# Performance work log

Measured on AMD Instinct MI355X. Metric: run time of the kernel, lower is better.

## Reference

```python
import math
import jax, jax.numpy as jnp
import numpy as np

NUM_HEADS = 16


def setup_inputs() -> dict:
    key = jax.random.key(0)
    ks = jax.random.split(key, 5)
    B, S, D = 2, 2048, 1024
    return {
        "x": jax.random.normal(ks[0], (B, S, D), dtype=jnp.float32),
        "w_in": jax.random.normal(ks[1], (3 * D, D), dtype=jnp.float32) * (1.0 / math.sqrt(D)),
        "b_in": jax.random.normal(ks[2], (3 * D,), dtype=jnp.float32) * 0.02,
        "w_out": jax.random.normal(ks[3], (D, D), dtype=jnp.float32) * (1.0 / math.sqrt(D)),
        "b_out": jax.random.normal(ks[4], (D,), dtype=jnp.float32) * 0.02,
        "causal_mask": 1,
    }


def reference(x, w_in, b_in, w_out, b_out, causal_mask):
    B, S, D = x.shape
    H = NUM_HEADS
    dh = D // H
    # in-projection: torch Linear -> x @ W^T + b, then chunk into q,k,v
    qkv = x @ w_in.T + b_in                      # [B,S,3D]
    q, k, v = jnp.split(qkv, 3, axis=-1)         # each [B,S,D]
    q = q.reshape(B, S, H, dh).transpose(0, 2, 1, 3)  # [B,H,S,dh]
    k = k.reshape(B, S, H, dh).transpose(0, 2, 1, 3)
    v = v.reshape(B, S, H, dh).transpose(0, 2, 1, 3)
    # NOTE: original computes k @ q^T => scores indexed [key, query]
    scores = jnp.einsum("bhkd,bhqd->bhkq", k, q) / math.sqrt(dh)  # [B,H,Sk,Sq]
    if causal_mask:
        # triu(1) on the [k,q] matrix: mask where q_index > k_index
        mask = jnp.triu(jnp.ones((S, S), dtype=bool), 1)
        scores = jnp.where(mask, -jnp.inf, scores)
    att = jax.nn.softmax(scores, axis=-1)        # softmax over query axis (faithful)
    out = jnp.einsum("bhkq,bhqd->bhkd", att, v)  # [B,H,S,dh]
    out = out.transpose(0, 2, 1, 3).reshape(B, S, D)
    return out @ w_out.T + b_out
```

## Files before the change

### kernel.cpp

```cpp
#include <hip/hip_runtime.h>

typedef unsigned short u16;
typedef short bfrag __attribute__((ext_vector_type(8)));
typedef float facc  __attribute__((ext_vector_type(4)));
typedef float f16x  __attribute__((ext_vector_type(16)));

__device__ __forceinline__ u16 f2bf(float f){
  union { float f; unsigned u; } v; v.f = f;
  unsigned r = v.u + 0x7fffu + ((v.u >> 16) & 1u);
  return (u16)(r >> 16);
}

__device__ __forceinline__ unsigned cvt_pk_bf16(float lo, float hi){
  unsigned d;
  asm("v_cvt_pk_bf16_f32 %0, %1, %2" : "=v"(d) : "v"(lo), "v"(hi));
  return d;
}

__device__ __forceinline__ void gl_lds16(const void* g, void* l){
  __builtin_amdgcn_global_load_lds(
      (const __attribute__((address_space(1))) unsigned int*)g,
      (__attribute__((address_space(3))) unsigned int*)l,
      16, 0, 0);
}

__global__ __launch_bounds__(256) void cvt3_kernel(
    const float* __restrict__ s0, u16* __restrict__ d0, int n0,
    const float* __restrict__ s1, u16* __restrict__ d1, int n1,
    const float* __restrict__ s2, u16* __restrict__ d2)
{
  int i = (blockIdx.x * 256 + threadIdx.x) * 4;
  const float* src; u16* dst;
  if (i < n0){ src = s0; dst = d0; }
  else if (i < n0 + n1){ src = s1; dst = d1; i -= n0; }
  else { src = s2; dst = d2; i -= n0 + n1; }
  float4 f = *(const float4*)(src + i);
  ushort4 o;
  o.x = f2bf(f.x); o.y = f2bf(f.y); o.z = f2bf(f.z); o.w = f2bf(f.w);
  *(ushort4*)(dst + i) = o;
}

__global__ __launch_bounds__(512, 2) void gemm8p_qkv(
    const u16* __restrict__ A, const u16* __restrict__ B,
    const float* __restrict__ bias, u16* __restrict__ qkv)
{
  __shared__ u16 lds[66048];
  const int tid = threadIdx.x, lane = tid & 63;
  const int w = tid >> 6, wm = w >> 2, wn = w & 3;
  const int cl = lane & 15, g8 = (lane >> 4) * 8, r0 = (lane >> 4) * 4;
  constexpr int K = 1024, NT = 16;

  const int bid = blockIdx.x;
  const int chunk = bid & 7, pos = bid >> 3;
  const int mt = (chunk >> 2) * 8 + pos / 3;
  const int nt = (chunk & 3) * 3 + pos % 3;
  const int m0 = mt * 256, n0 = nt * 256;

  facc acc[8][4];
  #pragma unroll
  for (int mi = 0; mi < 8; ++mi)
    #pragma unroll
    for (int ni = 0; ni < 4; ++ni) acc[mi][ni] = (facc){0.f, 0.f, 0.f, 0.f};

  int aoff[4][2], boff[2][2];
  #pragma unroll
  for (int mi2 = 0; mi2 < 4; ++mi2)
    #pragma unroll
    for (int ks = 0; ks < 2; ++ks){
      int r = (2 * mi2 + wm) * 16 + cl;
      int U = r * 128 + (ks * 32 + g8) * 2;
      aoff[mi2][ks] = (U ^ (((U >> 9) & 1) << 5)) >> 1;
    }
  #pragma unroll
  for (int ni2 = 0; ni2 < 2; ++ni2)
    #pragma unroll
    for (int ks = 0; ks < 2; ++ks){
      int rB = (4 * ni2 + wn) * 16 + cl;
      int U = rB * 128 + (ks * 32 + g8) * 2;
      boff[ni2][ks] = (U ^ (((U >> 9) & 1) << 5)) >> 1;
    }

  int srow[2], scol[2];
  #pragma unroll
  for (int c = 0; c < 2; ++c){
    int Bh = c * 8192 + tid * 16;
    int E = Bh ^ (((Bh >> 9) & 1) << 5);
    srow[c] = E >> 7; scol[c] = (E & 127) >> 1;
  }

  auto stageA = [&](int t, int h){
    const int k0 = (t < NT) ? t * 64 : 0;
    const int slot = ((2 * t + h) & 3) * 8192;
    #pragma unroll
    for (int c = 0; c < 2; ++c)
      gl_lds16(A + (size_t)(m0 + h * 128 + srow[c]) * K + k0 + scol[c],
               lds + slot + c * 4096 + w * 512);
  };
  auto stageB = [&](int t, int h){
    const int k0 = (t < NT) ? t * 64 : 0;
    const int slot = 32768 + ((2 * t + h) & 3) * 8192;
    #pragma unroll
    for (int c = 0; c < 2; ++c)
      gl_lds16(B + (size_t)(n0 + h * 128 + srow[c]) * K + k0 + scol[c],
               lds + slot + c * 4096 + w * 512);
  };

  stageA(0, 0); stageB(0, 0); stageA(0, 1); stageB(0, 1); stageA(1, 0); stageB(1, 0);

  bfrag af[4][2], bf[2][2];

  for (int j = 0; j < NT; ++j){
    const int sa0 = ((2 * j) & 3) * 8192,      sa1 = ((2 * j + 1) & 3) * 8192;
    const int sb0 = 32768 + ((2 * j) & 3) * 8192, sb1 = 32768 + ((2 * j + 1) & 3) * 8192;

    stageA(j + 1, 1);
    asm volatile("s_waitcnt vmcnt(8)" ::: "memory");
    __builtin_amdgcn_s_barrier();
    #pragma unroll
    for (int mi2 = 0; mi2 < 4; ++mi2)
      #pragma unroll
      for (int ks = 0; ks < 2; ++ks) af[mi2][ks] = *(const bfrag*)&lds[sa0 + aoff[mi2][ks]];
    #pragma unroll
    for (int ni2 = 0; ni2 < 2; ++ni2)
      #pragma unroll
      for (int ks = 0; ks < 2; ++ks) bf[ni2][ks] = *(const bfrag*)&lds[sb0 + boff[ni2][ks]];
    asm volatile("s_waitcnt lgkmcnt(0)" ::: "memory");
    __builtin_amdgcn_sched_barrier(0);
    __builtin_amdgcn_s_setprio(1);
    #pragma unroll
    for (int mi2 = 0; mi2 < 4; ++mi2)
      #pragma unroll
      for (int ni2 = 0; ni2 < 2; ++ni2)
        #pragma unroll
        for (int ks = 0; ks < 2; ++ks)
          acc[mi2][ni2] = __builtin_amdgcn_mfma_f32_16x16x32_bf16(af[mi2][ks], bf[ni2][ks], acc[mi2][ni2], 0, 0, 0);
    __builtin_amdgcn_s_setprio(0);
    __builtin_amdgcn_s_barrier();

    stageB(j + 1, 1);
    asm volatile("s_waitcnt vmcnt(6)" ::: "memory");
    __builtin_amdgcn_s_barrier();
    #pragma unroll
    for (int ni2 = 0; ni2 < 2; ++ni2)
      #pragma unroll
      for (int ks = 0; ks < 2; ++ks) bf[ni2][ks] = *(const bfrag*)&lds[sb1 + boff[ni2][ks]];
    asm volatile("s_waitcnt lgkmcnt(0)" ::: "memory");
    __builtin_amdgcn_sched_barrier(0);
    __builtin_amdgcn_s_setprio(1);
    #pragma unroll
    for (int mi2 = 0; mi2 < 4; ++mi2)
      #pragma unroll
      for (int ni2 = 0; ni2 < 2; ++ni2)
        #pragma unroll
        for (int ks = 0; ks < 2; ++ks)
          acc[mi2][2 + ni2] = __builtin_amdgcn_mfma_f32_16x16x32_bf16(af[mi2][ks], bf[ni2][ks], acc[mi2][2 + ni2], 0, 0, 0);
    __builtin_amdgcn_s_setprio(0);
    __builtin_amdgcn_s_barrier();

    #pragma unroll
    for (int mi2 = 0; mi2 < 4; ++mi2)
      #pragma unroll
      for (int ks = 0; ks < 2; ++ks) af[mi2][ks] = *(const bfrag*)&lds[sa1 + aoff[mi2][ks]];
    #pragma unroll
    for (int ni2 = 0; ni2 < 2; ++ni2)
      #pragma unroll
      for (int ks = 0; ks < 2; ++ks) bf[ni2][ks] = *(const bfrag*)&lds[sb0 + boff[ni2][ks]];
    stageA(j + 2, 0);
    __builtin_amdgcn_s_barrier();
    asm volatile("s_waitcnt lgkmcnt(0)" ::: "memory");
    __builtin_amdgcn_sched_barrier(0);
    __builtin_amdgcn_s_setprio(1);
    #pragma unroll
    for (int mi2 = 0; mi2 < 4; ++mi2)
      #pragma unroll
      for (int ni2 = 0; ni2 < 2; ++ni2)
        #pragma unroll
        for (int ks = 0; ks < 2; ++ks)
          acc[4 + mi2][ni2] = __builtin_amdgcn_mfma_f32_16x16x32_bf16(af[mi2][ks], bf[ni2][ks], acc[4 + mi2][ni2], 0, 0, 0);
    __builtin_amdgcn_s_setprio(0);
    __builtin_amdgcn_s_barrier();

    #pragma unroll
    for (int ni2 = 0; ni2 < 2; ++ni2)
      #pragma unroll
      for (int ks = 0; ks < 2; ++ks) bf[ni2][ks] = *(const bfrag*)&lds[sb1 + boff[ni2][ks]];
    stageB(j + 2, 0);
    __builtin_amdgcn_s_barrier();
    asm volatile("s_waitcnt lgkmcnt(0)" ::: "memory");
    __builtin_amdgcn_sched_barrier(0);
    __builtin_amdgcn_s_setprio(1);
    #pragma unroll
    for (int mi2 = 0; mi2 < 4; ++mi2)
      #pragma unroll
      for (int ni2 = 0; ni2 < 2; ++ni2)
        #pragma unroll
        for (int ks = 0; ks < 2; ++ks)
          acc[4 + mi2][2 + ni2] = __builtin_amdgcn_mfma_f32_16x16x32_bf16(af[mi2][ks], bf[ni2][ks], acc[4 + mi2][2 + ni2], 0, 0, 0);
    __builtin_amdgcn_s_setprio(0);
    __builtin_amdgcn_s_barrier();
  }
  __syncthreads();

  const int bb = m0 >> 11, s0q = m0 & 2047;
  if (n0 < 2048){
    #pragma unroll
    for (int mi = 0; mi < 8; ++mi){
      const int m = m0 + (2 * mi + wm) * 16 + r0;
      #pragma unroll
      for (int ni = 0; ni < 4; ++ni){
        const int n = n0 + (4 * ni + wn) * 16 + cl;
        const float bv = bias[n];
        const int part = n >> 10, rest = n & 1023;
        const int h = rest >> 6, d = rest & 63;
        #pragma unroll
        for (int jj = 0; jj < 4; ++jj){
          float v = acc[mi][ni][jj] + bv;
          if (part == 0) v *= 0.18033688011112042f;
          const int mm = m + jj;
          qkv[(size_t)part * 4194304 + (size_t)(((mm >> 11) * 16 + h) * 2048 + (mm & 2047)) * 64 + d] = f2bf(v);
        }
      }
    }
  } else {
    u16* tr = lds;
    const int h0 = (n0 - 2048) >> 6;
    #pragma unroll
    for (int mi = 0; mi < 8; ++mi){
      const int sl = (2 * mi + wm) * 16 + r0;
      #pragma unroll
      for (int ni = 0; ni < 4; ++ni){
        const float bv = bias[n0 + (4 * ni + wn) * 16 + cl];
        const int off = (ni * 64 + wn * 16 + cl) * 258 + sl;
        *(unsigned*)&tr[off]     = cvt_pk_bf16(acc[mi][ni][0] + bv, acc[mi][ni][1] + bv);
        *(unsigned*)&tr[off + 2] = cvt_pk_bf16(acc[mi][ni][2] + bv, acc[mi][ni][3] + bv);
      }
    }
    __syncthreads();
    u16* vt_base = qkv + (size_t)2 * 4194304;
    const int hh = tid >> 7, dd = (tid >> 1) & 63, hf = tid & 1;
    u16* dst = vt_base + ((size_t)((bb * 16 + h0 + hh) * 64 + dd)) * 2048 + s0q + hf * 128;
    const u16* srcr = &tr[(hh * 64 + dd) * 258 + hf * 128];
    #pragma unroll
    for (int k = 0; k < 16; ++k)
      *(uint4*)(dst + k * 8) = *(const uint4*)(srcr + k * 8);
  }
}

__device__ __forceinline__ void stage_tile(const u16* __restrict__ G, u16* lds,
                                           int row0, int k0, int K, int tid){
  #pragma unroll
  for (int c = 0; c < 2; ++c){
    int e = c * 2048 + tid * 8;
    int row = e >> 5, col = e & 31;
    gl_lds16(G + (size_t)(row0 + row) * K + k0 + col, lds + c * 2048 + (tid >> 6) * 512);
  }
}

__global__ __launch_bounds__(256) void gemm_out(
    const u16* __restrict__ A, const u16* __restrict__ B,
    const float* __restrict__ bias, float* __restrict__ Cf,
    int M, int N, int K)
{
  __shared__ u16 smem[16384];
  u16* Ash = smem;
  u16* Bsh = smem + 8192;
  const int tid = threadIdx.x, lane = tid & 63;
  const int w = tid >> 6, wm = w >> 1, wn = w & 1;
  const int cl = lane & 15, g8 = (lane >> 4) * 8;

  const int bid = blockIdx.x;
  const int chunk = bid & 7, pos = bid >> 3;
  const int mt = (chunk >> 1) * 8 + pos / 4;
  const int nt = (chunk & 1) * 4 + pos % 4;
  const int n0 = nt * 128, m0 = mt * 128;

  facc acc[4][4];
  #pragma unroll
  for (int mi = 0; mi < 4; ++mi)
    #pragma unroll
    for (int ni = 0; ni < 4; ++ni)
      acc[mi][ni] = (facc){0.f, 0.f, 0.f, 0.f};

  const int NT = K >> 5;
  stage_tile(A, Ash, m0, 0, K, tid);
  stage_tile(B, Bsh, n0, 0, K, tid);
  __syncthreads();
  int cur = 0;
  for (int kt = 0; kt < NT; ++kt){
    if (kt + 1 < NT){
      stage_tile(A, Ash + (cur ^ 1) * 4096, m0, (kt + 1) << 5, K, tid);
      stage_tile(B, Bsh + (cur ^ 1) * 4096, n0, (kt + 1) << 5, K, tid);
    }
    const u16* As = Ash + cur * 4096; const u16* Bs = Bsh + cur * 4096;
    bfrag af[4], bfr[4];
    #pragma unroll
    for (int mi = 0; mi < 4; ++mi)
      af[mi] = *(const bfrag*)&As[(wm * 64 + mi * 16 + cl) * 32 + g8];
    #pragma unroll
    for (int ni = 0; ni < 4; ++ni)
      bfr[ni] = *(const bfrag*)&Bs[(wn * 64 + ni * 16 + cl) * 32 + g8];
    #pragma unroll
    for (int mi = 0; mi < 4; ++mi)
      #pragma unroll
      for (int ni = 0; ni < 4; ++ni)
        acc[mi][ni] = __builtin_amdgcn_mfma_f32_16x16x32_bf16(af[mi], bfr[ni], acc[mi][ni], 0, 0, 0);
    __syncthreads();
    cur ^= 1;
  }

  const int r0 = (lane >> 4) * 4;
  #pragma unroll
  for (int mi = 0; mi < 4; ++mi){
    const int mbase = m0 + wm * 64 + mi * 16 + r0;
    #pragma unroll
    for (int ni = 0; ni < 4; ++ni){
      const int n = n0 + wn * 64 + ni * 16 + cl;
      const float bv = bias[n];
      #pragma unroll
      for (int j = 0; j < 4; ++j)
        Cf[(size_t)(mbase + j) * N + n] = acc[mi][ni][j] + bv;
    }
  }
}

template<int NSUB, bool MASK>
__device__ __forceinline__ void attn_tile(
    const u16* __restrict__ Kt, const u16* __restrict__ VTh, int jt,
    int il, int hi, const bfrag (&bq)[4],
    f16x& o0, f16x& o1, float& m_s, float& l_s)
{
  bfrag vf[NSUB * 4];
  #pragma unroll
  for (int sub = 0; sub < NSUB; ++sub)
    #pragma unroll
    for (int half = 0; half < 2; ++half){
      const int jcol = jt * 64 + sub * 32 + half * 16 + hi * 8;
      vf[sub * 4 + half * 2 + 0] = *(const bfrag*)(VTh + (size_t)il * 2048 + jcol);
      vf[sub * 4 + half * 2 + 1] = *(const bfrag*)(VTh + (size_t)(32 + il) * 2048 + jcol);
    }
  bfrag kf[NSUB * 4];
  #pragma unroll
  for (int sub = 0; sub < NSUB; ++sub)
    #pragma unroll
    for (int kt = 0; kt < 4; ++kt)
      kf[sub * 4 + kt] = *(const bfrag*)(Kt + (size_t)(sub * 32 + il) * 64 + kt * 16 + hi * 8);

  f16x s[NSUB];
  #pragma unroll
  for (int sub = 0; sub < NSUB; ++sub)
    #pragma unroll
    for (int r = 0; r < 16; ++r) s[sub][r] = 0.f;
  __builtin_amdgcn_s_setprio(1);
  #pragma unroll
  for (int kt = 0; kt < 4; ++kt)
    #pragma unroll
    for (int sub = 0; sub < NSUB; ++sub)
      s[sub] = __builtin_amdgcn_mfma_f32_32x32x16_bf16(kf[sub * 4 + kt], bq[kt], s[sub], 0, 0, 0);
  __builtin_amdgcn_s_setprio(0);

  if (MASK){
    #pragma unroll
    for (int r = 0; r < 16; ++r){
      const int qj = (r & 3) + 8 * (r >> 2) + 4 * hi;
      if (qj > il) s[NSUB - 1][r] = -1e30f;
    }
  }

  float tmax = -1e30f;
  #pragma unroll
  for (int sub = 0; sub < NSUB; ++sub){
    float a[8];
    #pragma unroll
    for (int e = 0; e < 8; ++e) a[e] = fmaxf(s[sub][e], s[sub][e + 8]);
    #pragma unroll
    for (int e = 0; e < 4; ++e) a[e] = fmaxf(a[e], a[e + 4]);
    a[0] = fmaxf(fmaxf(a[0], a[2]), fmaxf(a[1], a[3]));
    tmax = fmaxf(tmax, a[0]);
  }
  {
    auto tt = __builtin_amdgcn_permlane32_swap(__float_as_uint(tmax),
                                               __float_as_uint(tmax), false, false);
    tmax = fmaxf(__uint_as_float(tt[0]), __uint_as_float(tt[1]));
  }
  if (__any(tmax - m_s > 8.0f)){
    const float nm = fmaxf(m_s, tmax);
    const float sc = __builtin_amdgcn_exp2f(m_s - nm);
    m_s = nm; l_s *= sc;
    #pragma unroll
    for (int r = 0; r < 16; ++r){
      const float scb = __shfl(sc, (r & 3) + 8 * (r >> 2) + 4 * hi, 64);
      o0[r] *= scb; o1[r] *= scb;
    }
  }

  float rsum = 0.f;
  #pragma unroll
  for (int sub = 0; sub < NSUB; ++sub){
    #pragma unroll
    for (int r = 0; r < 16; ++r)
      s[sub][r] = __builtin_amdgcn_exp2f(s[sub][r] - m_s);
    float a[8];
    #pragma unroll
    for (int e = 0; e < 8; ++e) a[e] = s[sub][e] + s[sub][e + 8];
    #pragma unroll
    for (int e = 0; e < 4; ++e) a[e] = a[e] + a[e + 4];
    rsum += (a[0] + a[2]) + (a[1] + a[3]);
  }
  {
    auto rr = __builtin_amdgcn_permlane32_swap(__float_as_uint(rsum),
                                               __float_as_uint(rsum), false, false);
    rsum = __uint_as_float(rr[0]) + __uint_as_float(rr[1]);
  }
  l_s += rsum;

  #pragma unroll
  for (int sub = 0; sub < NSUB; ++sub)
    #pragma unroll
    for (int half = 0; half < 2; ++half){
      const int q0 = 8 * half;
      unsigned a0 = cvt_pk_bf16(s[sub][q0],     s[sub][q0 + 1]);
      unsigned a1 = cvt_pk_bf16(s[sub][q0 + 2], s[sub][q0 + 3]);
      unsigned b0 = cvt_pk_bf16(s[sub][q0 + 4], s[sub][q0 + 5]);
      unsigned b1 = cvt_pk_bf16(s[sub][q0 + 6], s[sub][q0 + 7]);
      auto r0p = __builtin_amdgcn_permlane32_swap(a0, b0, false, false);
      auto r1p = __builtin_amdgcn_permlane32_swap(a1, b1, false, false);
      union { bfrag f; unsigned u[4]; } pa;
      pa.u[0] = r0p[0]; pa.u[1] = r1p[0]; pa.u[2] = r0p[1]; pa.u[3] = r1p[1];

      __builtin_amdgcn_s_setprio(1);
      o0 = __builtin_amdgcn_mfma_f32_32x32x16_bf16(pa.f, vf[sub * 4 + half * 2 + 0], o0, 0, 0, 0);
      o1 = __builtin_amdgcn_mfma_f32_32x32x16_bf16(pa.f, vf[sub * 4 + half * 2 + 1], o1, 0, 0, 0);
      __builtin_amdgcn_s_setprio(0);
    }
}

__global__ __launch_bounds__(128, 3) void attn_kernel(
    const u16* __restrict__ qarr, const u16* __restrict__ karr,
    const u16* __restrict__ vtarr, u16* __restrict__ aout,
    const int* __restrict__ cmask)
{
  __shared__ float cO[32 * 64];
  __shared__ float cm0[32], cl0[32], cm1[32], cl1[32];
  const int tid = threadIdx.x, lane = tid & 63, w = tid >> 6;
  const int il = lane & 31, hi = lane >> 5;
  const int bh = blockIdx.x;
  const int jw = 63 - (int)blockIdx.y;
  const int iw = jw * 32;
  const u16* Qh  = karr  + (size_t)bh * 131072;
  const u16* Kh  = qarr  + (size_t)bh * 131072;
  const u16* VTh = vtarr + (size_t)bh * 131072;
  const bool do_mask = (cmask[0] != 0);

  bfrag bq[4];
  #pragma unroll
  for (int kt = 0; kt < 4; ++kt)
    bq[kt] = *(const bfrag*)(Qh + (size_t)(iw + il) * 64 + kt * 16 + hi * 8);

  f16x o0, o1;
  #pragma unroll
  for (int r = 0; r < 16; ++r){ o0[r] = 0.f; o1[r] = 0.f; }
  float m_s = -1e30f, l_s = 0.f;

  const int my_diag = jw >> 1;
  const int dsub    = jw & 1;
  const int lim = do_mask ? my_diag : 32;

  for (int jt = w; jt < lim; jt += 2)
    attn_tile<2, false>(Kh + (size_t)jt * 4096, VTh, jt, il, hi, bq, o0, o1, m_s, l_s);

  if (do_mask && (my_diag & 1) == w){
    if (dsub == 0)
      attn_tile<1, true>(Kh + (size_t)my_diag * 4096, VTh, my_diag, il, hi, bq, o0, o1, m_s, l_s);
    else
      attn_tile<2, true>(Kh + (size_t)my_diag * 4096, VTh, my_diag, il, hi, bq, o0, o1, m_s, l_s);
  }

  if (w == 1){
    #pragma unroll
    for (int r = 0; r < 16; ++r){
      const int row = (r & 3) + 8 * (r >> 2) + 4 * hi;
      cO[row * 64 + il]      = o0[r];
      cO[row * 64 + il + 32] = o1[r];
    }
    cm1[il] = m_s; cl1[il] = l_s;
  } else {
    cm0[il] = m_s; cl0[il] = l_s;
  }
  __syncthreads();
  if (w == 0){
    const int bb = bh >> 4, h = bh & 15;
    #pragma unroll
    for (int r = 0; r < 16; ++r){
      const int rl = (r & 3) + 8 * (r >> 2) + 4 * hi;
      const float mA = cm0[rl], mB = cm1[rl];
      const float lA = cl0[rl], lB = cl1[rl];
      const float M  = fmaxf(mA, mB);
      const float eA = __builtin_amdgcn_exp2f(mA - M);
      const float eB = __builtin_amdgcn_exp2f(mB - M);
      const float inv = 1.0f / (lA * eA + lB * eB);
      const float ob0 = cO[rl * 64 + il], ob1 = cO[rl * 64 + il + 32];
      u16* dst = aout + (size_t)(bb * 2048 + iw + rl) * 1024 + h * 64 + il;
      dst[0]  = f2bf((o0[r] * eA + ob0 * eB) * inv);
      dst[32] = f2bf((o1[r] * eA + ob1 * eB) * inv);
    }
  }
}

extern "C" void kernel_launch(void* const* d_in, const int* in_sizes, int n_in,
                              void* d_out, int out_size, void* d_ws, size_t ws_size,
                              hipStream_t stream)
{
  const float* x     = (const float*)d_in[0];
  const float* w_in  = (const float*)d_in[1];
  const float* b_in  = (const float*)d_in[2];
  const float* w_out = (const float*)d_in[3];
  const float* b_out = (const float*)d_in[4];
  const int*   cmask = (const int*)d_in[5];

  u16* ws     = (u16*)d_ws;
  u16* xb     = ws;
  u16* winb   = ws + 4194304;
  u16* woutb  = ws + 7340032;
  u16* qs     = ws + 8388608;
  u16* attn_o = ws + 20971520;

  cvt3_kernel<<<8192, 256, 0, stream>>>(x, xb, 4194304,
                                        w_in, winb, 3145728,
                                        w_out, woutb);

  gemm8p_qkv<<<192, 512, 0, stream>>>(xb, winb, b_in, qs);

  attn_kernel<<<dim3(32, 64), 128, 0, stream>>>(qs, qs + 4194304, qs + 8388608, attn_o, cmask);

  gemm_out<<<256, 256, 0, stream>>>(attn_o, woutb, b_out, (float*)d_out,
                                    4096, 1024, 1024);
}
```

Before: 146.9 us.

## Process two 32-row query stripes per attention block to reuse K/V fragments

Each attention block now handles 64 query rows, split into two 32-row stripes, instead of 32. Each K/V tile is loaded into registers once and used by both stripes, so global K/V traffic per query row is halved. The grid shrinks to 32x32 blocks, launch bounds are dropped, and register and LDS use per block grow, which may cut occupancy and parallelism. Causal load balance is also coarser, since each block's work now scales in 64-row steps.

```diff
diff --git a/kernel.cpp b/kernel.cpp
--- a/kernel.cpp
+++ b/kernel.cpp
@@ -110,7 +110,7 @@
   bfrag af[4][2], bf[2][2];
 
   for (int j = 0; j < NT; ++j){
-    const int sa0 = ((2 * j) & 3) * 8192,      sa1 = ((2 * j + 1) & 3) * 8192;
+    const int sa0 = ((2 * j) & 3) * 8192,         sa1 = ((2 * j + 1) & 3) * 8192;
     const int sb0 = 32768 + ((2 * j) & 3) * 8192, sb1 = 32768 + ((2 * j + 1) & 3) * 8192;
 
     stageA(j + 1, 1);
@@ -324,27 +324,11 @@
 }
 
 template<int NSUB, bool MASK>
-__device__ __forceinline__ void attn_tile(
-    const u16* __restrict__ Kt, const u16* __restrict__ VTh, int jt,
+__device__ __forceinline__ void stripe_body(
+    const bfrag (&kf)[8], const bfrag (&vf)[8],
     int il, int hi, const bfrag (&bq)[4],
     f16x& o0, f16x& o1, float& m_s, float& l_s)
 {
-  bfrag vf[NSUB * 4];
-  #pragma unroll
-  for (int sub = 0; sub < NSUB; ++sub)
-    #pragma unroll
-    for (int half = 0; half < 2; ++half){
-      const int jcol = jt * 64 + sub * 32 + half * 16 + hi * 8;
-      vf[sub * 4 + half * 2 + 0] = *(const bfrag*)(VTh + (size_t)il * 2048 + jcol);
-      vf[sub * 4 + half * 2 + 1] = *(const bfrag*)(VTh + (size_t)(32 + il) * 2048 + jcol);
-    }
-  bfrag kf[NSUB * 4];
-  #pragma unroll
-  for (int sub = 0; sub < NSUB; ++sub)
-    #pragma unroll
-    for (int kt = 0; kt < 4; ++kt)
-      kf[sub * 4 + kt] = *(const bfrag*)(Kt + (size_t)(sub * 32 + il) * 64 + kt * 16 + hi * 8);
-
   f16x s[NSUB];
   #pragma unroll
   for (int sub = 0; sub < NSUB; ++sub)
@@ -434,74 +418,104 @@
     }
 }
 
-__global__ __launch_bounds__(128, 3) void attn_kernel(
+__device__ __forceinline__ void load_tile(
+    bfrag (&kf)[8], bfrag (&vf)[8],
+    const u16* __restrict__ Kt, const u16* __restrict__ VTh, int jt, int il, int hi)
+{
+  #pragma unroll
+  for (int sub = 0; sub < 2; ++sub)
+    #pragma unroll
+    for (int half = 0; half < 2; ++half){
+      const int jcol = jt * 64 + sub * 32 + half * 16 + hi * 8;
+      vf[sub * 4 + half * 2 + 0] = *(const bfrag*)(VTh + (size_t)il * 2048 + jcol);
+      vf[sub * 4 + half * 2 + 1] = *(const bfrag*)(VTh + (size_t)(32 + il) * 2048 + jcol);
+    }
+  #pragma unroll
+  for (int sub = 0; sub < 2; ++sub)
+    #pragma unroll
+    for (int kt = 0; kt < 4; ++kt)
+      kf[sub * 4 + kt] = *(const bfrag*)(Kt + (size_t)(sub * 32 + il) * 64 + kt * 16 + hi * 8);
+}
+
+__global__ void attn_kernel(
     const u16* __restrict__ qarr, const u16* __restrict__ karr,
     const u16* __restrict__ vtarr, u16* __restrict__ aout,
     const int* __restrict__ cmask)
 {
-  __shared__ float cO[32 * 64];
-  __shared__ float cm0[32], cl0[32], cm1[32], cl1[32];
+  __shared__ float cO[64 * 64];
+  __shared__ float cm0[64], cl0[64], cm1[64], cl1[64];
   const int tid = threadIdx.x, lane = tid & 63, w = tid >> 6;
   const int il = lane & 31, hi = lane >> 5;
   const int bh = blockIdx.x;
-  const int jw = 63 - (int)blockIdx.y;
-  const int iw = jw * 32;
+  const int bi = 31 - (int)blockIdx.y;
+  const int i0 = bi * 64;
   const u16* Qh  = karr  + (size_t)bh * 131072;
   const u16* Kh  = qarr  + (size_t)bh * 131072;
   const u16* VTh = vtarr + (size_t)bh * 131072;
   const bool do_mask = (cmask[0] != 0);
 
-  bfrag bq[4];
-  #pragma unroll
-  for (int kt = 0; kt < 4; ++kt)
-    bq[kt] = *(const bfrag*)(Qh + (size_t)(iw + il) * 64 + kt * 16 + hi * 8);
-
-  f16x o0, o1;
-  #pragma unroll
-  for (int r = 0; r < 16; ++r){ o0[r] = 0.f; o1[r] = 0.f; }
-  float m_s = -1e30f, l_s = 0.f;
-
-  const int my_diag = jw >> 1;
-  const int dsub    = jw & 1;
-  const int lim = do_mask ? my_diag : 32;
-
-  for (int jt = w; jt < lim; jt += 2)
-    attn_tile<2, false>(Kh + (size_t)jt * 4096, VTh, jt, il, hi, bq, o0, o1, m_s, l_s);
-
-  if (do_mask && (my_diag & 1) == w){
-    if (dsub == 0)
-      attn_tile<1, true>(Kh + (size_t)my_diag * 4096, VTh, my_diag, il, hi, bq, o0, o1, m_s, l_s);
-    else
-      attn_tile<2, true>(Kh + (size_t)my_diag * 4096, VTh, my_diag, il, hi, bq, o0, o1, m_s, l_s);
+  bfrag bqL[4], bqH[4];
+  #pragma unroll
+  for (int kt = 0; kt < 4; ++kt){
+    bqL[kt] = *(const bfrag*)(Qh + (size_t)(i0 + il) * 64 + kt * 16 + hi * 8);
+    bqH[kt] = *(const bfrag*)(Qh + (size_t)(i0 + 32 + il) * 64 + kt * 16 + hi * 8);
+  }
+
+  f16x o0L, o1L, o0H, o1H;
+  #pragma unroll
+  for (int r = 0; r < 16; ++r){ o0L[r] = 0.f; o1L[r] = 0.f; o0H[r] = 0.f; o1H[r] = 0.f; }
+  float mL = -1e30f, lL = 0.f, mH = -1e30f, lH = 0.f;
+
+  const int lim = do_mask ? bi : 32;
+
+  bfrag kf[8], vf[8];
+  for (int jt = w; jt < lim; jt += 2){
+    load_tile(kf, vf, Kh + (size_t)jt * 4096, VTh, jt, il, hi);
+    stripe_body<2, false>(kf, vf, il, hi, bqL, o0L, o1L, mL, lL);
+    stripe_body<2, false>(kf, vf, il, hi, bqH, o0H, o1H, mH, lH);
+  }
+
+  if (do_mask && (bi & 1) == w){
+    load_tile(kf, vf, Kh + (size_t)bi * 4096, VTh, bi, il, hi);
+    stripe_body<1, true>(kf, vf, il, hi, bqL, o0L, o1L, mL, lL);
+    stripe_body<2, true>(kf, vf, il, hi, bqH, o0H, o1H, mH, lH);
   }
 
   if (w == 1){
     #pragma unroll
     for (int r = 0; r < 16; ++r){
       const int row = (r & 3) + 8 * (r >> 2) + 4 * hi;
-      cO[row * 64 + il]      = o0[r];
-      cO[row * 64 + il + 32] = o1[r];
-    }
-    cm1[il] = m_s; cl1[il] = l_s;
+      cO[row * 64 + il]             = o0L[r];
+      cO[row * 64 + il + 32]        = o1L[r];
+      cO[(32 + row) * 64 + il]      = o0H[r];
+      cO[(32 + row) * 64 + il + 32] = o1H[r];
+    }
+    cm1[il] = mL; cl1[il] = lL; cm1[32 + il] = mH; cl1[32 + il] = lH;
   } else {
-    cm0[il] = m_s; cl0[il] = l_s;
+    cm0[il] = mL; cl0[il] = lL; cm0[32 + il] = mH; cl0[32 + il] = lH;
   }
   __syncthreads();
   if (w == 0){
     const int bb = bh >> 4, h = bh & 15;
     #pragma unroll
-    for (int r = 0; r < 16; ++r){
-      const int rl = (r & 3) + 8 * (r >> 2) + 4 * hi;
-      const float mA = cm0[rl], mB = cm1[rl];
-      const float lA = cl0[rl], lB = cl1[rl];
-      const float M  = fmaxf(mA, mB);
-      const float eA = __builtin_amdgcn_exp2f(mA - M);
-      const float eB = __builtin_amdgcn_exp2f(mB - M);
-      const float inv = 1.0f / (lA * eA + lB * eB);
-      const float ob0 = cO[rl * 64 + il], ob1 = cO[rl * 64 + il + 32];
-      u16* dst = aout + (size_t)(bb * 2048 + iw + rl) * 1024 + h * 64 + il;
-      dst[0]  = f2bf((o0[r] * eA + ob0 * eB) * inv);
-      dst[32] = f2bf((o1[r] * eA + ob1 * eB) * inv);
+    for (int p = 0; p < 2; ++p){
+      #pragma unroll
+      for (int r = 0; r < 16; ++r){
+        const int rl = (r & 3) + 8 * (r >> 2) + 4 * hi;
+        const int sr = p * 32 + rl;
+        const float mA = cm0[sr], mB = cm1[sr];
+        const float lA = cl0[sr], lB = cl1[sr];
+        const float M  = fmaxf(mA, mB);
+        const float eA = __builtin_amdgcn_exp2f(mA - M);
+        const float eB = __builtin_amdgcn_exp2f(mB - M);
+        const float inv = 1.0f / (lA * eA + lB * eB);
+        const float ob0 = cO[sr * 64 + il], ob1 = cO[sr * 64 + il + 32];
+        const float a0 = (p ? o0H[r] : o0L[r]) * eA + ob0 * eB;
+        const float a1 = (p ? o1H[r] : o1L[r]) * eA + ob1 * eB;
+        u16* dst = aout + (size_t)(bb * 2048 + i0 + sr) * 1024 + h * 64 + il;
+        dst[0]  = f2bf(a0 * inv);
+        dst[32] = f2bf(a1 * inv);
+      }
     }
   }
 }
@@ -530,7 +544,7 @@
 
   gemm8p_qkv<<<192, 512, 0, stream>>>(xb, winb, b_in, qs);
 
-  attn_kernel<<<dim3(32, 64), 128, 0, stream>>>(qs, qs + 4194304, qs + 8388608, attn_o, cmask);
+  attn_kernel<<<dim3(32, 32), 128, 0, stream>>>(qs, qs + 4194304, qs + 8388608, attn_o, cmask);
 
   gemm_out<<<256, 256, 0, stream>>>(attn_o, woutb, b_out, (float*)d_out,
                                     4096, 1024, 1024);
```

After: 292.8 us. 1.99x slower.
